# Kernel optimization log

Hardware: AMD Instinct MI355X
Metric: run time of the kernel (lower is better)

## Reference

```python
import jax, jax.numpy as jnp
import numpy as np
from jax import lax

DN = ('NCHW', 'OIHW', 'NCHW')
BN_EPS = 1e-5
LRELU_SLOPE = 0.01


def conv_block(x, w1, b1, w2, b2, gamma, bn_bias):
    # Conv2d(512->256, k=1) -> Conv2d(256->512, k=3, pad=1) -> LeakyReLU -> BatchNorm2d(512)
    y = lax.conv_general_dilated(x, w1, (1, 1), 'VALID', dimension_numbers=DN)
    y = y + b1[None, :, None, None]
    y = lax.conv_general_dilated(y, w2, (1, 1), 'SAME', dimension_numbers=DN)
    y = y + b2[None, :, None, None]
    y = jnp.where(y > 0, y, LRELU_SLOPE * y)
    # BatchNorm2d in training mode: batch statistics over (B, H, W) per channel
    mean = jnp.mean(y, axis=(0, 2, 3))
    var = jnp.var(y, axis=(0, 2, 3))
    y = (y - mean[None, :, None, None]) * lax.rsqrt(var + BN_EPS)[None, :, None, None]
    return y * gamma[None, :, None, None] + bn_bias[None, :, None, None]


def setup_inputs() -> dict:
    key = jax.random.key(0)
    ks = jax.random.split(key, 9)
    B, C, H, W = 8, 512, 32, 32
    x = jax.random.normal(ks[0], (B, C, H, W), dtype=jnp.float32)
    x1 = jax.random.normal(ks[1], (B, C, H, W), dtype=jnp.float32)
    x2 = jax.random.normal(ks[2], (B, C, H, W), dtype=jnp.float32)
    w1 = jax.random.normal(ks[3], (256, 512, 1, 1), dtype=jnp.float32) * 0.02
    b1 = jnp.zeros((256,), dtype=jnp.float32)
    w2 = jax.random.normal(ks[4], (512, 256, 3, 3), dtype=jnp.float32) * 0.02
    b2 = jnp.zeros((512,), dtype=jnp.float32)
    gamma = jnp.ones((512,), dtype=jnp.float32)
    bn_bias = jnp.zeros((512,), dtype=jnp.float32)
    beta = jax.random.normal(ks[5], (1,), dtype=jnp.float32)  # Parameter(zeros(1)) in torch; random so output is non-trivial
    return {"x": x, "x1": x1, "x2": x2, "w1": w1, "b1": b1, "w2": w2,
            "b2": b2, "gamma": gamma, "bn_bias": bn_bias, "beta": beta}


def reference(x, x1, x2, w1, b1, w2, b2, gamma, bn_bias, beta):
    B, C, H, W = x1.shape
    N = H * W
    F1 = conv_block(x1, w1, b1, w2, b2, gamma, bn_bias).reshape(B, C, N)   # [B, C, N]
    F2 = conv_block(x2, w1, b1, w2, b2, gamma, bn_bias).reshape(B, C, N)   # [B, C, N]
    scores = jnp.einsum('bcn,bdn->bcd', F1, F2)                            # [B, C, C]
    attention = jax.nn.softmax(scores, axis=-1)
    out = jnp.einsum('bcd,bdn->bcn', attention, x.reshape(B, C, N))
    return beta * out.reshape(B, C, H, W)
```

## Files before the change

kernel.cpp:

```cpp
#include <hip/hip_runtime.h>


typedef __attribute__((ext_vector_type(8))) short bfrag;
typedef __attribute__((ext_vector_type(4))) float facc;

__device__ __forceinline__ unsigned short bf16_rn(float v) {
  unsigned u = __float_as_uint(v);
  return (unsigned short)((u + 0x7fffu + ((u >> 16) & 1u)) >> 16);
}

__device__ __forceinline__ void dma16(const void* g, const void* lds) {
  __builtin_amdgcn_global_load_lds(
      (const __attribute__((address_space(1))) unsigned int*)g,
      (__attribute__((address_space(3))) unsigned int*)(unsigned int)(unsigned long long)(const char*)lds,
      16, 0, 0);
}

__global__ __launch_bounds__(256) void prologue(
    const float* __restrict__ x1, const float* __restrict__ x2,
    const float* __restrict__ w2, unsigned char* __restrict__ x12timg,
    unsigned short* __restrict__ w2s, float* __restrict__ statsz) {
  int bid = blockIdx.x;
  int t = threadIdx.x;
  if (bid < 8192) {
    __shared__ float tile[32][33];
    int p0 = (bid & 31) * 32, ci0 = ((bid >> 5) & 15) * 32, z = bid >> 9;
    const float* src = (z < 8) ? x1 + (size_t)z * 524288 : x2 + (size_t)(z - 8) * 524288;
    {
      int ci_l = t >> 5, p_l = t & 31;
#pragma unroll
      for (int j = 0; j < 4; j++)
        tile[ci_l + 8 * j][p_l] = src[(size_t)(ci0 + ci_l + 8 * j) * 1024 + p0 + p_l];
    }
    __syncthreads();
    {
      int p_l = t >> 3, cg = (t & 7) * 4;
      unsigned short hh[4], ll[4];
#pragma unroll
      for (int j = 0; j < 4; j++) {
        float v = tile[cg + j][p_l];
        hh[j] = bf16_rn(v);
        ll[j] = bf16_rn(v - __uint_as_float((unsigned)hh[j] << 16));
      }
      int px = p0 + p_l, row = px & 127, panel = px >> 7;
      int c = ci0 + cg, kc = c >> 6, ck = (c >> 3) & 7;
      int slot = ck ^ (row & 7);
      size_t byte = (((size_t)(z * 8 + panel) * 8 + kc) * 128 + row) * 256 + slot * 16 + (c & 7) * 2;
      *(ushort4*)(x12timg + byte) = make_ushort4(hh[0], hh[1], hh[2], hh[3]);
      *(ushort4*)(x12timg + byte + 128) = make_ushort4(ll[0], ll[1], ll[2], ll[3]);
    }
  } else {
    int co = bid - 8192;
    if (co < 40) statsz[co * 256 + t] = 0.f;
    int panel = co >> 7, w = (co >> 5) & 3, j = (co >> 4) & 1, lm = co & 15;
    int chunk = t >> 5, q = (t >> 3) & 3, e = t & 7;
    int lane = q * 16 + lm;
    const float* src = w2 + ((size_t)co * 256 + t) * 9;
#pragma unroll
    for (int tap = 0; tap < 9; tap++) {
      float v = src[tap];
      unsigned short h = bf16_rn(v);
      unsigned short l = bf16_rn(v - __uint_as_float((unsigned)h << 16));
      int P = (panel * 8 + chunk) * 9 + tap;
      size_t us = (size_t)P * 8192 + w * 2048 + j * 1024 + lane * 8 + e;
      w2s[us] = h;
      w2s[us + 512] = l;
    }
  }
}

__global__ __launch_bounds__(256) void transpose_split_x(
    const float* __restrict__ x, unsigned char* __restrict__ img) {
  __shared__ float tile[32][33];
  int z = blockIdx.z;
  const float* src = x + (size_t)z * 524288;
  int ci0 = blockIdx.y * 32, p0 = blockIdx.x * 32;
  int t = threadIdx.x;
  {
    int ci_l = t >> 5, p_l = t & 31;
#pragma unroll
    for (int j = 0; j < 4; j++)
      tile[ci_l + 8 * j][p_l] = src[(size_t)(ci0 + ci_l + 8 * j) * 1024 + p0 + p_l];
  }
  __syncthreads();
  {
    int p_l = t >> 3, cg = (t & 7) * 4;
    unsigned short hh[4], ll[4];
#pragma unroll
    for (int j = 0; j < 4; j++) {
      float v = tile[cg + j][p_l];
      hh[j] = bf16_rn(v);
      ll[j] = bf16_rn(v - __uint_as_float((unsigned)hh[j] << 16));
    }
    int px = p0 + p_l, row = px & 127, panel = px >> 7;
    int c = ci0 + cg, kc = c >> 6, ck = (c >> 3) & 7;
    int slot = ck ^ (row & 7);
    size_t byte = (((size_t)(z * 8 + panel) * 8 + kc) * 128 + row) * 256 + slot * 16 + (c & 7) * 2;
    *(ushort4*)(img + byte) = make_ushort4(hh[0], hh[1], hh[2], hh[3]);
    *(ushort4*)(img + byte + 128) = make_ushort4(ll[0], ll[1], ll[2], ll[3]);
  }
}

template <int KTOT, int EPI, int AF32, int KSPLIT>
__global__ __launch_bounds__(256, 2) void gemm_nt(
    const void* __restrict__ Asrc, long long aZS, int aKC,
    const unsigned char* __restrict__ Bimg, long long bZS, int bKC,
    void* __restrict__ out0,
    const float* __restrict__ p0, const float* __restrict__ p1,
    const float* __restrict__ p2, const float* __restrict__ p3) {
  __shared__ __attribute__((aligned(16))) unsigned char smem[49152];
  int t = threadIdx.x;
  int z = blockIdx.z;
  int zb = z, kh = 0;
  if (KSPLIT) { zb = z & 7; kh = z >> 3; }
  int m0 = blockIdx.y * 128, n0 = blockIdx.x * 64;
  int w = t >> 6, lane = t & 63;
  int lm = lane & 15, q = lane >> 4;
  int mh = (w & 1) * 64, nh = (w >> 1) * 32;
  const unsigned char* Abase = (const unsigned char*)Asrc + (size_t)zb * aZS +
      (size_t)(m0 >> 7) * ((size_t)aKC << 15) + (size_t)w * 8192 + (size_t)lane * 16;
  const unsigned char* Bbase = Bimg + (size_t)zb * bZS +
      (size_t)(n0 >> 7) * ((size_t)bKC << 15) + (size_t)(n0 & 127) * 256 +
      (size_t)w * 4096 + (size_t)lane * 16;
  facc acc[4][2] = {};
  for (int k0 = 0; k0 < KTOT; k0 += 64) {
    int kc = (KSPLIT ? kh * (KTOT / 64) : 0) + (k0 >> 6);
    __syncthreads();
    if (AF32) {
      const float* Af = (const float*)Asrc;
#pragma unroll
      for (int j = 0; j < 8; j++) {
        int idx = t + 256 * j;
        int row = idx >> 4, c4 = idx & 15;
        float4 v = *(const float4*)(Af + (size_t)(m0 + row) * KTOT + k0 + c4 * 4);
        unsigned short h0 = bf16_rn(v.x), h1 = bf16_rn(v.y), h2 = bf16_rn(v.z), h3 = bf16_rn(v.w);
        unsigned short l0 = bf16_rn(v.x - __uint_as_float((unsigned)h0 << 16));
        unsigned short l1 = bf16_rn(v.y - __uint_as_float((unsigned)h1 << 16));
        unsigned short l2 = bf16_rn(v.z - __uint_as_float((unsigned)h2 << 16));
        unsigned short l3 = bf16_rn(v.w - __uint_as_float((unsigned)h3 << 16));
        int base = row * 256 + (((c4 >> 1) ^ (row & 7)) * 16) + (c4 & 1) * 8;
        *(ushort4*)(smem + base) = make_ushort4(h0, h1, h2, h3);
        *(ushort4*)(smem + base + 128) = make_ushort4(l0, l1, l2, l3);
      }
    } else {
      const unsigned char* ap = Abase + ((size_t)kc << 15);
#pragma unroll
      for (int j = 0; j < 8; j++) dma16(ap + j * 1024, smem + w * 8192 + j * 1024);
    }
    {
      const unsigned char* bp = Bbase + ((size_t)kc << 15);
#pragma unroll
      for (int j = 0; j < 4; j++) dma16(bp + j * 1024, smem + 32768 + w * 4096 + j * 1024);
    }
    __syncthreads();
#pragma unroll
    for (int ks = 0; ks < 2; ks++) {
      bfrag ah[4], al[4], bh[2], bl[2];
#pragma unroll
      for (int mt = 0; mt < 4; mt++) {
        int m = mh + mt * 16 + lm;
        int phys = ((ks * 4 + q) ^ (m & 7)) * 16;
        const unsigned char* p = smem + m * 256 + phys;
        ah[mt] = *(const bfrag*)p;
        al[mt] = *(const bfrag*)(p + 128);
      }
#pragma unroll
      for (int nt = 0; nt < 2; nt++) {
        int n = nh + nt * 16 + lm;
        int phys = ((ks * 4 + q) ^ (n & 7)) * 16;
        const unsigned char* p = smem + 32768 + n * 256 + phys;
        bh[nt] = *(const bfrag*)p;
        bl[nt] = *(const bfrag*)(p + 128);
      }
#pragma unroll
      for (int mt = 0; mt < 4; mt++)
#pragma unroll
        for (int nt = 0; nt < 2; nt++) {
          acc[mt][nt] = __builtin_amdgcn_mfma_f32_16x16x32_bf16(ah[mt], bh[nt], acc[mt][nt], 0, 0, 0);
          acc[mt][nt] = __builtin_amdgcn_mfma_f32_16x16x32_bf16(ah[mt], bl[nt], acc[mt][nt], 0, 0, 0);
          acc[mt][nt] = __builtin_amdgcn_mfma_f32_16x16x32_bf16(al[mt], bh[nt], acc[mt][nt], 0, 0, 0);
        }
    }
  }
  if (EPI == 0) {
    unsigned char* Yimg = (unsigned char*)out0;
    int g = zb;
#pragma unroll
    for (int mt = 0; mt < 4; mt++) {
      int mb = m0 + mh + mt * 16 + q * 4;
      int ch = mb >> 5, chunk = (mb >> 3) & 3, e2 = (mb & 7) * 2;
#pragma unroll
      for (int nt = 0; nt < 2; nt++) {
        int px = n0 + nh + nt * 16 + lm;
        int gy = px >> 5, gx = px & 31;
        int slot = chunk ^ ((gx + 1) & 7);
        size_t base = ((size_t)((g * 8 + ch) * 32 + gy)) * 4096 + gx * 128 + slot * 16 + e2;
        unsigned short hh[4], ll[4];
#pragma unroll
        for (int r = 0; r < 4; r++) {
          float v = acc[mt][nt][r] + p0[mb + r];
          hh[r] = bf16_rn(v);
          ll[r] = bf16_rn(v - __uint_as_float((unsigned)hh[r] << 16));
        }
        *(ushort4*)(Yimg + base) = make_ushort4(hh[0], hh[1], hh[2], hh[3]);
        *(ushort4*)(Yimg + (base ^ 64)) = make_ushort4(ll[0], ll[1], ll[2], ll[3]);
      }
    }
  } else if (EPI == 1) {
    float* S = (float*)out0 + (size_t)kh * 2097152;
    const float* stats = p0;
    const float* rowsum = p1;
    const float* gamma = p2;
    const float* bnb = p3;
    float a2v[2], t2v[2], r2v[2];
#pragma unroll
    for (int nt = 0; nt < 2; nt++) {
      int d = n0 + nh + nt * 16 + lm;
      float mu = stats[512 + d] * (1.f / 8192.f);
      float var = stats[1536 + d] * (1.f / 8192.f) - mu * mu;
      float a = gamma[d] * rsqrtf(var + 1e-5f);
      a2v[nt] = a;
      t2v[nt] = bnb[d] - mu * a;
      r2v[nt] = rowsum[(8 + zb) * 512 + d];
    }
#pragma unroll
    for (int mt = 0; mt < 4; mt++)
#pragma unroll
      for (int r = 0; r < 4; r++) {
        int cc = m0 + mh + mt * 16 + q * 4 + r;
        float mu = stats[cc] * (1.f / 8192.f);
        float var = stats[1024 + cc] * (1.f / 8192.f) - mu * mu;
        float a1 = gamma[cc] * rsqrtf(var + 1e-5f);
        float t1 = bnb[cc] - mu * a1;
        float r1 = rowsum[zb * 512 + cc];
#pragma unroll
        for (int nt = 0; nt < 2; nt++) {
          int d = n0 + nh + nt * 16 + lm;
          float sc = a1 * a2v[nt] * acc[mt][nt][r];
          if (kh == 0)
            sc += a1 * t2v[nt] * r1 + t1 * a2v[nt] * r2v[nt] + 1024.f * t1 * t2v[nt];
          S[((size_t)(zb * 512 + cc)) * 512 + d] = sc;
        }
      }
  } else {
    float* O = (float*)out0;
    float sc = p0[0];
#pragma unroll
    for (int mt = 0; mt < 4; mt++)
#pragma unroll
      for (int r = 0; r < 4; r++) {
        int cc = m0 + mh + mt * 16 + q * 4 + r;
#pragma unroll
        for (int nt = 0; nt < 2; nt++) {
          int n = n0 + nh + nt * 16 + lm;
          O[((size_t)(zb * 512 + cc)) * 1024 + n] = sc * acc[mt][nt][r];
        }
      }
  }
}

__global__ __launch_bounds__(256, 4) void conv3x3_mfma(
    const unsigned char* __restrict__ Yimg, const unsigned short* __restrict__ w2s,
    const float* __restrict__ b2, unsigned char* __restrict__ Fimg,
    float* __restrict__ stats, float* __restrict__ rowsum) {
  __shared__ __attribute__((aligned(16))) unsigned char smem[26112];
  int t = threadIdx.x;
  int g = blockIdx.z;
  int panel = blockIdx.y;
  int co_base = panel * 128;
  int y0 = blockIdx.x * 2;
  int w = t >> 6, lane = t & 63;
  int lm = lane & 15, q = lane >> 4;
  const unsigned char* w2sb = (const unsigned char*)w2s +
      (((size_t)panel * 72) << 14) + (size_t)w * 4096 + (size_t)lane * 16;
  auto stageStrip = [&](int slot, int gy, int cc) {
    unsigned char* dst = smem + slot * 4352 + 128 + w * 1024;
    if ((unsigned)gy < 32u) {
      const unsigned char* srcp = Yimg +
          ((size_t)((g * 8 + cc) * 32 + gy)) * 4096 + w * 1024 + lane * 16;
      dma16(srcp, dst);
    } else {
      *(uint4*)(dst + lane * 16) = make_uint4(0u, 0u, 0u, 0u);
    }
  };
  for (int u = t; u < 1632; u += 256)
    *(uint4*)(smem + (size_t)u * 16) = make_uint4(0u, 0u, 0u, 0u);
  __syncthreads();
  stageStrip(0, y0 - 1, 0);
  stageStrip(1, y0 + 0, 0);
  stageStrip(2, y0 + 1, 0);
  stageStrip(3, y0 + 2, 0);
  __syncthreads();
  facc acc[2][4] = {};
#pragma unroll 1
  for (int c = 0; c < 8; c++) {
    int base4 = (c * 4) % 6;
#pragma unroll 1
    for (int tap = 0; tap < 9; tap++) {
      int dy = tap / 3, dx = tap - dy * 3;
      const unsigned char* wp = w2sb + (((size_t)(c * 9 + tap)) << 14);
      bfrag wh[2], wl[2];
#pragma unroll
      for (int j = 0; j < 2; j++) {
        wh[j] = *(const bfrag*)(wp + j * 2048);
        wl[j] = *(const bfrag*)(wp + j * 2048 + 1024);
      }
      if (c < 7) {
        if (tap == 0) {
          int p4 = base4 + 4; p4 = p4 < 6 ? p4 : p4 - 6;
          int p5 = base4 + 5; p5 = p5 < 6 ? p5 : p5 - 6;
          stageStrip(p4, y0 - 1, c + 1);
          stageStrip(p5, y0 + 0, c + 1);
        } else if (tap == 3) {
          stageStrip(base4, y0 + 1, c + 1);
        } else if (tap == 6) {
          stageStrip(base4 + 1, y0 + 2, c + 1);
        }
      }
      int bd = base4 + dy;
      int r0 = bd < 6 ? bd : bd - 6;
      int r1 = bd + 1 < 6 ? bd + 1 : bd - 5;
      bfrag bh[4], bl[4];
#pragma unroll
      for (int i = 0; i < 4; i++) {
        int xh = (i & 1) * 16 + lm + dx;
        int slot = (i >> 1) ? r1 : r0;
        const unsigned char* pb = smem + slot * 4352 + xh * 128;
        int ph = (q ^ (xh & 7)) * 16;
        bh[i] = *(const bfrag*)(pb + ph);
        bl[i] = *(const bfrag*)(pb + (ph ^ 64));
      }
#pragma unroll
      for (int j = 0; j < 2; j++)
#pragma unroll
        for (int i = 0; i < 4; i++) {
          acc[j][i] = __builtin_amdgcn_mfma_f32_16x16x32_bf16(wh[j], bh[i], acc[j][i], 0, 0, 0);
          acc[j][i] = __builtin_amdgcn_mfma_f32_16x16x32_bf16(wh[j], bl[i], acc[j][i], 0, 0, 0);
          acc[j][i] = __builtin_amdgcn_mfma_f32_16x16x32_bf16(wl[j], bh[i], acc[j][i], 0, 0, 0);
        }
      __syncthreads();
    }
  }
  int grp = g >> 3;
  int px0 = blockIdx.x * 64;
#pragma unroll
  for (int j = 0; j < 2; j++) {
#pragma unroll
    for (int r = 0; r < 4; r++) {
      int co = co_base + w * 32 + j * 16 + q * 4 + r;
      int row = co & 127;
      float bb = b2[co];
      float s = 0.f, s2 = 0.f;
#pragma unroll
      for (int i = 0; i < 4; i++) {
        float v = acc[j][i][r] + bb;
        v = v > 0.f ? v : 0.01f * v;
        unsigned short h = bf16_rn(v);
        unsigned short l = bf16_rn(v - __uint_as_float((unsigned)h << 16));
        int px = px0 + i * 16 + lm;
        int kc = px >> 6, ck = (px >> 3) & 7;
        int slot = ck ^ (row & 7);
        size_t byte = (((size_t)(g * 4 + panel) * 16 + kc) * 128 + row) * 256 +
                      slot * 16 + (px & 7) * 2;
        *(unsigned short*)(Fimg + byte) = h;
        *(unsigned short*)(Fimg + byte + 128) = l;
        s += v;
        s2 = fmaf(v, v, s2);
      }
#pragma unroll
      for (int d = 1; d <= 8; d <<= 1) {
        s += __shfl_xor(s, d);
        s2 += __shfl_xor(s2, d);
      }
      if (lm == 0) {
        atomicAdd(&stats[grp * 512 + co], s);
        atomicAdd(&stats[1024 + grp * 512 + co], s2);
        atomicAdd(&rowsum[g * 512 + co], s);
      }
    }
  }
}

__global__ __launch_bounds__(256) void softmax_rows(const float* __restrict__ S,
                                                    unsigned char* __restrict__ attimg) {
  int rowg = blockIdx.x;
  int z = rowg >> 9, c = rowg & 511;
  const float* p = S + (size_t)rowg * 512;
  const float* p1 = p + 2097152;
  int t = threadIdx.x;
  float2 va = *(const float2*)(p + 2 * t);
  float2 vb = *(const float2*)(p1 + 2 * t);
  float vx = va.x + vb.x, vy = va.y + vb.y;
  float mx = fmaxf(vx, vy);
#pragma unroll
  for (int d = 32; d >= 1; d >>= 1) mx = fmaxf(mx, __shfl_xor(mx, d));
  __shared__ float sred[8];
  int wave = t >> 6, lane = t & 63;
  if (lane == 0) sred[wave] = mx;
  __syncthreads();
  float m4 = fmaxf(fmaxf(sred[0], sred[1]), fmaxf(sred[2], sred[3]));
  float ex = expf(vx - m4), ey = expf(vy - m4);
  float s = ex + ey;
#pragma unroll
  for (int d = 32; d >= 1; d >>= 1) s += __shfl_xor(s, d);
  if (lane == 0) sred[4 + wave] = s;
  __syncthreads();
  float inv = 1.f / (sred[4] + sred[5] + sred[6] + sred[7]);
  float px_ = ex * inv, py_ = ey * inv;
  unsigned short h0 = bf16_rn(px_), h1 = bf16_rn(py_);
  unsigned short l0 = bf16_rn(px_ - __uint_as_float((unsigned)h0 << 16));
  unsigned short l1 = bf16_rn(py_ - __uint_as_float((unsigned)h1 << 16));
  int rowl = c & 127, panel = c >> 7;
  int d0 = 2 * t;
  int kc = d0 >> 6, ck = (d0 >> 3) & 7;
  int slot = ck ^ (rowl & 7);
  size_t byte = (((size_t)(z * 4 + panel) * 8 + kc) * 128 + rowl) * 256 +
                slot * 16 + (d0 & 7) * 2;
  *(ushort2*)(attimg + byte) = make_ushort2(h0, h1);
  *(ushort2*)(attimg + byte + 128) = make_ushort2(l0, l1);
}

extern "C" void kernel_launch(void* const* d_in, const int* in_sizes, int n_in,
                              void* d_out, int out_size, void* d_ws, size_t ws_size,
                              hipStream_t stream) {
  const float* x = (const float*)d_in[0];
  const float* x1 = (const float*)d_in[1];
  const float* x2 = (const float*)d_in[2];
  const float* w1 = (const float*)d_in[3];
  const float* b1 = (const float*)d_in[4];
  const float* w2 = (const float*)d_in[5];
  const float* b2 = (const float*)d_in[6];
  const float* gamma = (const float*)d_in[7];
  const float* bnb = (const float*)d_in[8];
  const float* beta = (const float*)d_in[9];
  float* out = (float*)d_out;
  unsigned char* wsb = (unsigned char*)d_ws;

  unsigned char* x12timg = wsb;
  unsigned char* Fimg = wsb;
  unsigned char* xtimg = wsb;
  unsigned char* attimg = wsb + 16777216;
  unsigned char* Yimg = wsb + 33554432;
  float* S = (float*)(wsb + 33554432);
  unsigned short* w2s = (unsigned short*)(wsb + 50331648);
  float* stats = (float*)(wsb + 55050240);
  float* rowsum = (float*)(wsb + 55058432);

  prologue<<<8704, 256, 0, stream>>>(x1, x2, w2, x12timg, w2s, stats);
  gemm_nt<512, 0, 1, 0><<<dim3(16, 2, 16), 256, 0, stream>>>(
      w1, 0LL, 0, x12timg, 2097152LL, 8, Yimg, b1, nullptr, nullptr, nullptr);
  conv3x3_mfma<<<dim3(16, 4, 16), 256, 0, stream>>>(
      Yimg, w2s, b2, Fimg, stats, rowsum);
  gemm_nt<512, 1, 0, 1><<<dim3(8, 4, 16), 256, 0, stream>>>(
      Fimg, 2097152LL, 16, Fimg + (size_t)8 * 2097152, 2097152LL, 16,
      S, stats, rowsum, gamma, bnb);
  transpose_split_x<<<dim3(32, 16, 8), 256, 0, stream>>>(x, xtimg);
  softmax_rows<<<4096, 256, 0, stream>>>(S, attimg);
  gemm_nt<512, 2, 0, 0><<<dim3(16, 4, 8), 256, 0, stream>>>(
      attimg, 1048576LL, 8, xtimg, 2097152LL, 8, out, beta, nullptr, nullptr, nullptr);
}
```

Before: 291.8 us.

## Switch conv3x3 to 32x32x16 MFMA and sync once per kernel row

The 3x3 convolution kernel moves from 16x16x32 bf16 MFMA tiles to 32x32x16 tiles. The prologue re-lays out the split weights to match the new operand fragments, and the epilogue index mapping and shuffle reduction are updated. The tap loop is restructured so the block synchronises once per kernel row (dy) instead of once per tap, which cuts barriers by a factor of three. This is meant to reduce LDS fragment loads and issue overhead per FLOP, at the cost of more accumulator registers and a more complex weight layout.

```diff
diff --git a/kernel.cpp b/kernel.cpp
--- a/kernel.cpp
+++ b/kernel.cpp
@@ -3,6 +3,7 @@
 
 typedef __attribute__((ext_vector_type(8))) short bfrag;
 typedef __attribute__((ext_vector_type(4))) float facc;
+typedef __attribute__((ext_vector_type(16))) float facc16;
 
 __device__ __forceinline__ unsigned short bf16_rn(float v) {
   unsigned u = __float_as_uint(v);
@@ -52,9 +53,9 @@
   } else {
     int co = bid - 8192;
     if (co < 40) statsz[co * 256 + t] = 0.f;
-    int panel = co >> 7, w = (co >> 5) & 3, j = (co >> 4) & 1, lm = co & 15;
-    int chunk = t >> 5, q = (t >> 3) & 3, e = t & 7;
-    int lane = q * 16 + lm;
+    int panel = co >> 7, w = (co >> 5) & 3, r31 = co & 31;
+    int chunk = t >> 5, kh = (t >> 4) & 1, l5 = (t >> 3) & 1, e = t & 7;
+    int lane = l5 * 32 + r31;
     const float* src = w2 + ((size_t)co * 256 + t) * 9;
 #pragma unroll
     for (int tap = 0; tap < 9; tap++) {
@@ -62,7 +63,7 @@
       unsigned short h = bf16_rn(v);
       unsigned short l = bf16_rn(v - __uint_as_float((unsigned)h << 16));
       int P = (panel * 8 + chunk) * 9 + tap;
-      size_t us = (size_t)P * 8192 + w * 2048 + j * 1024 + lane * 8 + e;
+      size_t us = (size_t)P * 8192 + w * 2048 + kh * 1024 + lane * 8 + e;
       w2s[us] = h;
       w2s[us + 512] = l;
     }
@@ -270,7 +271,7 @@
   int co_base = panel * 128;
   int y0 = blockIdx.x * 2;
   int w = t >> 6, lane = t & 63;
-  int lm = lane & 15, q = lane >> 4;
+  int gx = lane & 31, l5 = lane >> 5;
   const unsigned char* w2sb = (const unsigned char*)w2s +
       (((size_t)panel * 72) << 14) + (size_t)w * 4096 + (size_t)lane * 16;
   auto stageStrip = [&](int slot, int gy, int cc) {
@@ -290,93 +291,92 @@
   stageStrip(1, y0 + 0, 0);
   stageStrip(2, y0 + 1, 0);
   stageStrip(3, y0 + 2, 0);
-  __syncthreads();
-  facc acc[2][4] = {};
+  facc16 acc[2] = {};
 #pragma unroll 1
   for (int c = 0; c < 8; c++) {
     int base4 = (c * 4) % 6;
 #pragma unroll 1
-    for (int tap = 0; tap < 9; tap++) {
-      int dy = tap / 3, dx = tap - dy * 3;
-      const unsigned char* wp = w2sb + (((size_t)(c * 9 + tap)) << 14);
-      bfrag wh[2], wl[2];
-#pragma unroll
-      for (int j = 0; j < 2; j++) {
-        wh[j] = *(const bfrag*)(wp + j * 2048);
-        wl[j] = *(const bfrag*)(wp + j * 2048 + 1024);
-      }
+    for (int dy = 0; dy < 3; dy++) {
+      __syncthreads();
       if (c < 7) {
-        if (tap == 0) {
+        if (dy == 0) {
           int p4 = base4 + 4; p4 = p4 < 6 ? p4 : p4 - 6;
           int p5 = base4 + 5; p5 = p5 < 6 ? p5 : p5 - 6;
           stageStrip(p4, y0 - 1, c + 1);
           stageStrip(p5, y0 + 0, c + 1);
-        } else if (tap == 3) {
+        } else if (dy == 1) {
           stageStrip(base4, y0 + 1, c + 1);
-        } else if (tap == 6) {
+        } else {
           stageStrip(base4 + 1, y0 + 2, c + 1);
         }
       }
       int bd = base4 + dy;
       int r0 = bd < 6 ? bd : bd - 6;
       int r1 = bd + 1 < 6 ? bd + 1 : bd - 5;
-      bfrag bh[4], bl[4];
-#pragma unroll
-      for (int i = 0; i < 4; i++) {
-        int xh = (i & 1) * 16 + lm + dx;
-        int slot = (i >> 1) ? r1 : r0;
-        const unsigned char* pb = smem + slot * 4352 + xh * 128;
-        int ph = (q ^ (xh & 7)) * 16;
-        bh[i] = *(const bfrag*)(pb + ph);
-        bl[i] = *(const bfrag*)(pb + (ph ^ 64));
-      }
-#pragma unroll
-      for (int j = 0; j < 2; j++)
-#pragma unroll
-        for (int i = 0; i < 4; i++) {
-          acc[j][i] = __builtin_amdgcn_mfma_f32_16x16x32_bf16(wh[j], bh[i], acc[j][i], 0, 0, 0);
-          acc[j][i] = __builtin_amdgcn_mfma_f32_16x16x32_bf16(wh[j], bl[i], acc[j][i], 0, 0, 0);
-          acc[j][i] = __builtin_amdgcn_mfma_f32_16x16x32_bf16(wl[j], bh[i], acc[j][i], 0, 0, 0);
-        }
-      __syncthreads();
+#pragma unroll
+      for (int dx = 0; dx < 3; dx++) {
+        const unsigned char* wp = w2sb + (((size_t)(c * 9 + dy * 3 + dx)) << 14);
+        bfrag wh[2], wl[2];
+#pragma unroll
+        for (int kh = 0; kh < 2; kh++) {
+          wh[kh] = *(const bfrag*)(wp + kh * 2048);
+          wl[kh] = *(const bfrag*)(wp + kh * 2048 + 1024);
+        }
+        int xh = gx + dx;
+        bfrag bh[2][2], bl[2][2];
+#pragma unroll
+        for (int i = 0; i < 2; i++) {
+          const unsigned char* pb = smem + (i ? r1 : r0) * 4352 + xh * 128;
+#pragma unroll
+          for (int kh = 0; kh < 2; kh++) {
+            int ph = ((kh * 2 + l5) ^ (xh & 7)) * 16;
+            bh[i][kh] = *(const bfrag*)(pb + ph);
+            bl[i][kh] = *(const bfrag*)(pb + (ph ^ 64));
+          }
+        }
+#pragma unroll
+        for (int i = 0; i < 2; i++)
+#pragma unroll
+          for (int kh = 0; kh < 2; kh++) {
+            acc[i] = __builtin_amdgcn_mfma_f32_32x32x16_bf16(wh[kh], bh[i][kh], acc[i], 0, 0, 0);
+            acc[i] = __builtin_amdgcn_mfma_f32_32x32x16_bf16(wh[kh], bl[i][kh], acc[i], 0, 0, 0);
+            acc[i] = __builtin_amdgcn_mfma_f32_32x32x16_bf16(wl[kh], bh[i][kh], acc[i], 0, 0, 0);
+          }
+      }
     }
   }
   int grp = g >> 3;
-  int px0 = blockIdx.x * 64;
-#pragma unroll
-  for (int j = 0; j < 2; j++) {
-#pragma unroll
-    for (int r = 0; r < 4; r++) {
-      int co = co_base + w * 32 + j * 16 + q * 4 + r;
-      int row = co & 127;
-      float bb = b2[co];
-      float s = 0.f, s2 = 0.f;
-#pragma unroll
-      for (int i = 0; i < 4; i++) {
-        float v = acc[j][i][r] + bb;
-        v = v > 0.f ? v : 0.01f * v;
-        unsigned short h = bf16_rn(v);
-        unsigned short l = bf16_rn(v - __uint_as_float((unsigned)h << 16));
-        int px = px0 + i * 16 + lm;
-        int kc = px >> 6, ck = (px >> 3) & 7;
-        int slot = ck ^ (row & 7);
-        size_t byte = (((size_t)(g * 4 + panel) * 16 + kc) * 128 + row) * 256 +
-                      slot * 16 + (px & 7) * 2;
-        *(unsigned short*)(Fimg + byte) = h;
-        *(unsigned short*)(Fimg + byte + 128) = l;
-        s += v;
-        s2 = fmaf(v, v, s2);
-      }
-#pragma unroll
-      for (int d = 1; d <= 8; d <<= 1) {
-        s += __shfl_xor(s, d);
-        s2 += __shfl_xor(s2, d);
-      }
-      if (lm == 0) {
-        atomicAdd(&stats[grp * 512 + co], s);
-        atomicAdd(&stats[1024 + grp * 512 + co], s2);
-        atomicAdd(&rowsum[g * 512 + co], s);
-      }
+#pragma unroll
+  for (int r = 0; r < 16; r++) {
+    int co = co_base + w * 32 + (r & 3) + 8 * (r >> 2) + 4 * l5;
+    int row = co & 127;
+    float bb = b2[co];
+    float s = 0.f, s2 = 0.f;
+#pragma unroll
+    for (int i = 0; i < 2; i++) {
+      float v = acc[i][r] + bb;
+      v = v > 0.f ? v : 0.01f * v;
+      unsigned short h = bf16_rn(v);
+      unsigned short l = bf16_rn(v - __uint_as_float((unsigned)h << 16));
+      int px = (y0 + i) * 32 + gx;
+      int kc = px >> 6, ck = (px >> 3) & 7;
+      int slot = ck ^ (row & 7);
+      size_t byte = (((size_t)(g * 4 + panel) * 16 + kc) * 128 + row) * 256 +
+                    slot * 16 + (px & 7) * 2;
+      *(unsigned short*)(Fimg + byte) = h;
+      *(unsigned short*)(Fimg + byte + 128) = l;
+      s += v;
+      s2 = fmaf(v, v, s2);
+    }
+#pragma unroll
+    for (int d = 1; d <= 16; d <<= 1) {
+      s += __shfl_xor(s, d);
+      s2 += __shfl_xor(s2, d);
+    }
+    if (gx == 0) {
+      atomicAdd(&stats[grp * 512 + co], s);
+      atomicAdd(&stats[1024 + grp * 512 + co], s2);
+      atomicAdd(&rowsum[g * 512 + co], s);
     }
   }
 }
```

Result: slower. 321.0 us (+10.0%).

## Remap conv3x3 warp tiling to 64 channels by 32 pixels per wave

Applied to the files above, without the earlier changes.

Each wave in the 3x3 conv MFMA kernel previously covered 32 output channels across 64 pixels (two image rows). It now covers 64 channels across 32 pixels (one row). The w2 prepacking layout changes to match, so each wave loads 8 weight fragments and 2 pixel fragment pairs per tap instead of 4 and 4. This trades global weight loads for fewer LDS reads, and it changes the register footprint and the cache reuse of weights across waves.

```diff
diff --git a/kernel.cpp b/kernel.cpp
--- a/kernel.cpp
+++ b/kernel.cpp
@@ -52,9 +52,9 @@
   } else {
     int co = bid - 8192;
     if (co < 40) statsz[co * 256 + t] = 0.f;
-    int panel = co >> 7, w = (co >> 5) & 3, j = (co >> 4) & 1, lm = co & 15;
-    int chunk = t >> 5, q = (t >> 3) & 3, e = t & 7;
-    int lane = q * 16 + lm;
+    int panel = co >> 7, coh = (co >> 6) & 1, jf = (co >> 4) & 3, lmv = co & 15;
+    int chunk = t >> 5, qv = (t >> 3) & 3, e = t & 7;
+    int lanev = qv * 16 + lmv;
     const float* src = w2 + ((size_t)co * 256 + t) * 9;
 #pragma unroll
     for (int tap = 0; tap < 9; tap++) {
@@ -62,7 +62,7 @@
       unsigned short h = bf16_rn(v);
       unsigned short l = bf16_rn(v - __uint_as_float((unsigned)h << 16));
       int P = (panel * 8 + chunk) * 9 + tap;
-      size_t us = (size_t)P * 8192 + w * 2048 + j * 1024 + lane * 8 + e;
+      size_t us = (((size_t)(P * 2 + coh) * 8 + jf * 2) * 512) + lanev * 8 + e;
       w2s[us] = h;
       w2s[us + 512] = l;
     }
@@ -271,8 +271,9 @@
   int y0 = blockIdx.x * 2;
   int w = t >> 6, lane = t & 63;
   int lm = lane & 15, q = lane >> 4;
-  const unsigned char* w2sb = (const unsigned char*)w2s +
-      (((size_t)panel * 72) << 14) + (size_t)w * 4096 + (size_t)lane * 16;
+  int coh = w & 1, pxh = w >> 1;
+  const unsigned char* wg0 = (const unsigned char*)w2s +
+      (((size_t)panel * 72) << 14) + (size_t)coh * 8192 + (size_t)lane * 16;
   auto stageStrip = [&](int slot, int gy, int cc) {
     unsigned char* dst = smem + slot * 4352 + 128 + w * 1024;
     if ((unsigned)gy < 32u) {
@@ -291,20 +292,17 @@
   stageStrip(2, y0 + 1, 0);
   stageStrip(3, y0 + 2, 0);
   __syncthreads();
-  facc acc[2][4] = {};
+  facc acc[4][2] = {};
 #pragma unroll 1
   for (int c = 0; c < 8; c++) {
     int base4 = (c * 4) % 6;
 #pragma unroll 1
     for (int tap = 0; tap < 9; tap++) {
       int dy = tap / 3, dx = tap - dy * 3;
-      const unsigned char* wp = w2sb + (((size_t)(c * 9 + tap)) << 14);
-      bfrag wh[2], wl[2];
-#pragma unroll
-      for (int j = 0; j < 2; j++) {
-        wh[j] = *(const bfrag*)(wp + j * 2048);
-        wl[j] = *(const bfrag*)(wp + j * 2048 + 1024);
-      }
+      const unsigned char* wp = wg0 + (((size_t)(c * 9 + tap)) << 14);
+      bfrag W[8];
+#pragma unroll
+      for (int u = 0; u < 8; u++) W[u] = *(const bfrag*)(wp + u * 1024);
       if (c < 7) {
         if (tap == 0) {
           int p4 = base4 + 4; p4 = p4 < 6 ? p4 : p4 - 6;
@@ -317,26 +315,24 @@
           stageStrip(base4 + 1, y0 + 2, c + 1);
         }
       }
-      int bd = base4 + dy;
-      int r0 = bd < 6 ? bd : bd - 6;
-      int r1 = bd + 1 < 6 ? bd + 1 : bd - 5;
-      bfrag bh[4], bl[4];
-#pragma unroll
-      for (int i = 0; i < 4; i++) {
-        int xh = (i & 1) * 16 + lm + dx;
-        int slot = (i >> 1) ? r1 : r0;
-        const unsigned char* pb = smem + slot * 4352 + xh * 128;
+      int bd = base4 + dy + pxh;
+      int rs = bd < 6 ? bd : bd - 6;
+      bfrag bh[2], bl[2];
+#pragma unroll
+      for (int i = 0; i < 2; i++) {
+        int xh = i * 16 + lm + dx;
+        const unsigned char* pb = smem + rs * 4352 + xh * 128;
         int ph = (q ^ (xh & 7)) * 16;
         bh[i] = *(const bfrag*)(pb + ph);
         bl[i] = *(const bfrag*)(pb + (ph ^ 64));
       }
 #pragma unroll
-      for (int j = 0; j < 2; j++)
-#pragma unroll
-        for (int i = 0; i < 4; i++) {
-          acc[j][i] = __builtin_amdgcn_mfma_f32_16x16x32_bf16(wh[j], bh[i], acc[j][i], 0, 0, 0);
-          acc[j][i] = __builtin_amdgcn_mfma_f32_16x16x32_bf16(wh[j], bl[i], acc[j][i], 0, 0, 0);
-          acc[j][i] = __builtin_amdgcn_mfma_f32_16x16x32_bf16(wl[j], bh[i], acc[j][i], 0, 0, 0);
+      for (int j = 0; j < 4; j++)
+#pragma unroll
+        for (int i = 0; i < 2; i++) {
+          acc[j][i] = __builtin_amdgcn_mfma_f32_16x16x32_bf16(W[2 * j], bh[i], acc[j][i], 0, 0, 0);
+          acc[j][i] = __builtin_amdgcn_mfma_f32_16x16x32_bf16(W[2 * j], bl[i], acc[j][i], 0, 0, 0);
+          acc[j][i] = __builtin_amdgcn_mfma_f32_16x16x32_bf16(W[2 * j + 1], bh[i], acc[j][i], 0, 0, 0);
         }
       __syncthreads();
     }
@@ -344,20 +340,20 @@
   int grp = g >> 3;
   int px0 = blockIdx.x * 64;
 #pragma unroll
-  for (int j = 0; j < 2; j++) {
+  for (int j = 0; j < 4; j++) {
 #pragma unroll
     for (int r = 0; r < 4; r++) {
-      int co = co_base + w * 32 + j * 16 + q * 4 + r;
+      int co = co_base + coh * 64 + j * 16 + q * 4 + r;
       int row = co & 127;
       float bb = b2[co];
       float s = 0.f, s2 = 0.f;
 #pragma unroll
-      for (int i = 0; i < 4; i++) {
+      for (int i = 0; i < 2; i++) {
         float v = acc[j][i][r] + bb;
         v = v > 0.f ? v : 0.01f * v;
         unsigned short h = bf16_rn(v);
         unsigned short l = bf16_rn(v - __uint_as_float((unsigned)h << 16));
-        int px = px0 + i * 16 + lm;
+        int px = px0 + pxh * 32 + i * 16 + lm;
         int kc = px >> 6, ck = (px >> 3) & 7;
         int slot = ck ^ (row & 7);
         size_t byte = (((size_t)(g * 4 + panel) * 16 + kc) * 128 + row) * 256 +
```

New measurement: 332.8 us. 14.0% more time.

## Software-pipeline conv3x3 MFMA loop with double-buffered weight and LDS fragments

Applied to the files above, without the earlier changes.

Unrolls the 8x9 channel-chunk/tap loop of the 3x3 conv into a macro-generated sequence. Weight fragments and LDS input fragments for the next tap are loaded into a second register set while MFMAs run on the current set. Scheduling barriers keep the loads ahead of the MFMAs, and a raw s_barrier replaces __syncthreads. A dummy DMA in the zero-padding path keeps outstanding load counts uniform. Occupancy is lowered from 4 to 3 blocks to make room for the extra registers, and the c<7 staging guard is dropped, so the final chunk issues harmless out-of-range prefetches.

```diff
diff --git a/kernel.cpp b/kernel.cpp
--- a/kernel.cpp
+++ b/kernel.cpp
@@ -259,11 +259,63 @@
   }
 }
 
-__global__ __launch_bounds__(256, 4) void conv3x3_mfma(
+#define PREFETCH_W(Wh_, Wl_, CARG, TAPN)                                       \
+  {                                                                            \
+    const unsigned char* wp_ = w2sb + (((size_t)((CARG)*9 + (TAPN))) << 14);   \
+    _Pragma("unroll") for (int j_ = 0; j_ < 2; j_++) {                         \
+      Wh_[j_] = *(const bfrag*)(wp_ + j_ * 2048);                              \
+      Wl_[j_] = *(const bfrag*)(wp_ + j_ * 2048 + 1024);                       \
+    }                                                                          \
+  }
+#define PREFETCH_B(Bh_, Bl_, CARG, TAPN)                                       \
+  {                                                                            \
+    const int dyn_ = (TAPN) / 3, dxn_ = (TAPN) % 3;                            \
+    int bd_ = (((CARG)*4) % 6) + dyn_;                                         \
+    int r0_ = bd_ < 6 ? bd_ : bd_ - 6;                                         \
+    int r1_ = bd_ + 1 < 6 ? bd_ + 1 : bd_ - 5;                                 \
+    _Pragma("unroll") for (int i_ = 0; i_ < 4; i_++) {                         \
+      int xh_ = (i_ & 1) * 16 + lm + dxn_;                                     \
+      int slot_ = (i_ >> 1) ? r1_ : r0_;                                       \
+      const unsigned char* pb_ = smem + slot_ * 4352 + xh_ * 128;              \
+      int ph_ = (q ^ (xh_ & 7)) * 16;                                          \
+      Bh_[i_] = *(const bfrag*)(pb_ + ph_);                                    \
+      Bl_[i_] = *(const bfrag*)(pb_ + (ph_ ^ 64));                             \
+    }                                                                          \
+  }
+#define STAGE_SCHED(TAPTHIS, CTHIS, B4)                                        \
+  if ((TAPTHIS) == 0) {                                                        \
+    int p4_ = (B4) + 4; p4_ = p4_ < 6 ? p4_ : p4_ - 6;                         \
+    int p5_ = (B4) + 5; p5_ = p5_ < 6 ? p5_ : p5_ - 6;                         \
+    stageStrip(p4_, y0 - 1, (CTHIS) + 1);                                      \
+    stageStrip(p5_, y0 + 0, (CTHIS) + 1);                                      \
+  } else if ((TAPTHIS) == 3) {                                                 \
+    stageStrip((B4), y0 + 1, (CTHIS) + 1);                                     \
+  } else if ((TAPTHIS) == 6) {                                                 \
+    stageStrip((B4) + 1, y0 + 2, (CTHIS) + 1);                                 \
+  }
+#define MFMA_ON(Wh_, Wl_, Bh_, Bl_)                                            \
+  _Pragma("unroll") for (int j_ = 0; j_ < 2; j_++)                             \
+      _Pragma("unroll") for (int i_ = 0; i_ < 4; i_++) {                       \
+    acc[j_][i_] = __builtin_amdgcn_mfma_f32_16x16x32_bf16(Wh_[j_], Bh_[i_], acc[j_][i_], 0, 0, 0); \
+    acc[j_][i_] = __builtin_amdgcn_mfma_f32_16x16x32_bf16(Wh_[j_], Bl_[i_], acc[j_][i_], 0, 0, 0); \
+    acc[j_][i_] = __builtin_amdgcn_mfma_f32_16x16x32_bf16(Wl_[j_], Bh_[i_], acc[j_][i_], 0, 0, 0); \
+  }
+#define CONVBODY(WhC, WlC, BhC, BlC, WhN, WlN, BhN, BlN, B4, CTHIS, CNEXT, TAPTHIS, TAPNEXT) \
+  {                                                                            \
+    PREFETCH_W(WhN, WlN, CNEXT, TAPNEXT)                                       \
+    STAGE_SCHED(TAPTHIS, CTHIS, B4)                                            \
+    PREFETCH_B(BhN, BlN, CNEXT, TAPNEXT)                                       \
+    __builtin_amdgcn_sched_barrier(0);                                         \
+    MFMA_ON(WhC, WlC, BhC, BlC)                                                \
+    __builtin_amdgcn_sched_barrier(0);                                         \
+    __builtin_amdgcn_s_barrier();                                              \
+  }
+
+__global__ __launch_bounds__(256, 3) void conv3x3_mfma(
     const unsigned char* __restrict__ Yimg, const unsigned short* __restrict__ w2s,
     const float* __restrict__ b2, unsigned char* __restrict__ Fimg,
     float* __restrict__ stats, float* __restrict__ rowsum) {
-  __shared__ __attribute__((aligned(16))) unsigned char smem[26112];
+  __shared__ __attribute__((aligned(16))) unsigned char smem[30208];
   int t = threadIdx.x;
   int g = blockIdx.z;
   int panel = blockIdx.y;
@@ -273,73 +325,52 @@
   int lm = lane & 15, q = lane >> 4;
   const unsigned char* w2sb = (const unsigned char*)w2s +
       (((size_t)panel * 72) << 14) + (size_t)w * 4096 + (size_t)lane * 16;
-  auto stageStrip = [&](int slot, int gy, int cc) {
+  auto stageStrip = [&](int slot, int gy, int cc2) {
     unsigned char* dst = smem + slot * 4352 + 128 + w * 1024;
     if ((unsigned)gy < 32u) {
       const unsigned char* srcp = Yimg +
-          ((size_t)((g * 8 + cc) * 32 + gy)) * 4096 + w * 1024 + lane * 16;
+          ((size_t)((g * 8 + cc2) * 32 + gy)) * 4096 + w * 1024 + lane * 16;
       dma16(srcp, dst);
     } else {
       *(uint4*)(dst + lane * 16) = make_uint4(0u, 0u, 0u, 0u);
+      dma16(Yimg + w * 1024 + lane * 16, smem + 26112 + w * 1024);
     }
   };
   for (int u = t; u < 1632; u += 256)
     *(uint4*)(smem + (size_t)u * 16) = make_uint4(0u, 0u, 0u, 0u);
   __syncthreads();
+  bfrag WhA[2], WlA[2], BhA[4], BlA[4], WhB[2], WlB[2], BhB[4], BlB[4];
   stageStrip(0, y0 - 1, 0);
   stageStrip(1, y0 + 0, 0);
   stageStrip(2, y0 + 1, 0);
   stageStrip(3, y0 + 2, 0);
-  __syncthreads();
+  PREFETCH_W(WhA, WlA, 0, 0)
+  asm volatile("s_waitcnt vmcnt(4)" ::: "memory");
+  __builtin_amdgcn_s_barrier();
+  PREFETCH_B(BhA, BlA, 0, 0)
   facc acc[2][4] = {};
 #pragma unroll 1
-  for (int c = 0; c < 8; c++) {
-    int base4 = (c * 4) % 6;
-#pragma unroll 1
-    for (int tap = 0; tap < 9; tap++) {
-      int dy = tap / 3, dx = tap - dy * 3;
-      const unsigned char* wp = w2sb + (((size_t)(c * 9 + tap)) << 14);
-      bfrag wh[2], wl[2];
-#pragma unroll
-      for (int j = 0; j < 2; j++) {
-        wh[j] = *(const bfrag*)(wp + j * 2048);
-        wl[j] = *(const bfrag*)(wp + j * 2048 + 1024);
-      }
-      if (c < 7) {
-        if (tap == 0) {
-          int p4 = base4 + 4; p4 = p4 < 6 ? p4 : p4 - 6;
-          int p5 = base4 + 5; p5 = p5 < 6 ? p5 : p5 - 6;
-          stageStrip(p4, y0 - 1, c + 1);
-          stageStrip(p5, y0 + 0, c + 1);
-        } else if (tap == 3) {
-          stageStrip(base4, y0 + 1, c + 1);
-        } else if (tap == 6) {
-          stageStrip(base4 + 1, y0 + 2, c + 1);
-        }
-      }
-      int bd = base4 + dy;
-      int r0 = bd < 6 ? bd : bd - 6;
-      int r1 = bd + 1 < 6 ? bd + 1 : bd - 5;
-      bfrag bh[4], bl[4];
-#pragma unroll
-      for (int i = 0; i < 4; i++) {
-        int xh = (i & 1) * 16 + lm + dx;
-        int slot = (i >> 1) ? r1 : r0;
-        const unsigned char* pb = smem + slot * 4352 + xh * 128;
-        int ph = (q ^ (xh & 7)) * 16;
-        bh[i] = *(const bfrag*)(pb + ph);
-        bl[i] = *(const bfrag*)(pb + (ph ^ 64));
-      }
-#pragma unroll
-      for (int j = 0; j < 2; j++)
-#pragma unroll
-        for (int i = 0; i < 4; i++) {
-          acc[j][i] = __builtin_amdgcn_mfma_f32_16x16x32_bf16(wh[j], bh[i], acc[j][i], 0, 0, 0);
-          acc[j][i] = __builtin_amdgcn_mfma_f32_16x16x32_bf16(wh[j], bl[i], acc[j][i], 0, 0, 0);
-          acc[j][i] = __builtin_amdgcn_mfma_f32_16x16x32_bf16(wl[j], bh[i], acc[j][i], 0, 0, 0);
-        }
-      __syncthreads();
-    }
+  for (int cc = 0; cc < 4; cc++) {
+    int c0 = cc * 2, c1 = c0 + 1;
+    int b40 = (c0 * 4) % 6, b41 = (c1 * 4) % 6;
+    CONVBODY(WhA, WlA, BhA, BlA, WhB, WlB, BhB, BlB, b40, c0, c0, 0, 1)
+    CONVBODY(WhB, WlB, BhB, BlB, WhA, WlA, BhA, BlA, b40, c0, c0, 1, 2)
+    CONVBODY(WhA, WlA, BhA, BlA, WhB, WlB, BhB, BlB, b40, c0, c0, 2, 3)
+    CONVBODY(WhB, WlB, BhB, BlB, WhA, WlA, BhA, BlA, b40, c0, c0, 3, 4)
+    CONVBODY(WhA, WlA, BhA, BlA, WhB, WlB, BhB, BlB, b40, c0, c0, 4, 5)
+    CONVBODY(WhB, WlB, BhB, BlB, WhA, WlA, BhA, BlA, b40, c0, c0, 5, 6)
+    CONVBODY(WhA, WlA, BhA, BlA, WhB, WlB, BhB, BlB, b40, c0, c0, 6, 7)
+    CONVBODY(WhB, WlB, BhB, BlB, WhA, WlA, BhA, BlA, b40, c0, c0, 7, 8)
+    CONVBODY(WhA, WlA, BhA, BlA, WhB, WlB, BhB, BlB, b40, c0, c1, 8, 0)
+    CONVBODY(WhB, WlB, BhB, BlB, WhA, WlA, BhA, BlA, b41, c1, c1, 0, 1)
+    CONVBODY(WhA, WlA, BhA, BlA, WhB, WlB, BhB, BlB, b41, c1, c1, 1, 2)
+    CONVBODY(WhB, WlB, BhB, BlB, WhA, WlA, BhA, BlA, b41, c1, c1, 2, 3)
+    CONVBODY(WhA, WlA, BhA, BlA, WhB, WlB, BhB, BlB, b41, c1, c1, 3, 4)
+    CONVBODY(WhB, WlB, BhB, BlB, WhA, WlA, BhA, BlA, b41, c1, c1, 4, 5)
+    CONVBODY(WhA, WlA, BhA, BlA, WhB, WlB, BhB, BlB, b41, c1, c1, 5, 6)
+    CONVBODY(WhB, WlB, BhB, BlB, WhA, WlA, BhA, BlA, b41, c1, c1, 6, 7)
+    CONVBODY(WhA, WlA, BhA, BlA, WhB, WlB, BhB, BlB, b41, c1, c1, 7, 8)
+    CONVBODY(WhB, WlB, BhB, BlB, WhA, WlA, BhA, BlA, b41, c1, c1 + 1, 8, 0)
   }
   int grp = g >> 3;
   int px0 = blockIdx.x * 64;
```

After: 421.5 us. 44.4% more time.
